# Optimization experiments

Hardware: AMD Instinct MI355X
Metric: run time of the kernel (lower is better)

The kernel has to match this reference:

```python
import jax, jax.numpy as jnp
import numpy as np

C = 1024
GROUPS = 32
EPS = 1e-5
K = 20


def group_norm(v, weight, bias):
    # v: [B, C]; normalize per group of C//GROUPS channels (torch GroupNorm on 2D input)
    B = v.shape[0]
    g = v.reshape(B, GROUPS, C // GROUPS)
    mean = g.mean(axis=-1, keepdims=True)
    var = g.var(axis=-1, keepdims=True)
    g = (g - mean) * jax.lax.rsqrt(var + EPS)
    return g.reshape(B, C) * weight + bias


def setup_inputs() -> dict:
    key = jax.random.key(0)
    ks = jax.random.split(key, 16)
    B, L = 32, 2048
    s = 1.0 / np.sqrt(C)
    inp = {
        "x": jax.random.normal(ks[0], (B, L, C), dtype=jnp.float32),
        "W": jax.random.uniform(ks[1], (C, C), jnp.float32, -s, s),
        "b": jax.random.uniform(ks[2], (C,), jnp.float32, -s, s),
        "W1": jax.random.uniform(ks[3], (C, C), jnp.float32, -s, s),
        "b1": jax.random.uniform(ks[4], (C,), jnp.float32, -s, s),
        "Wm": jax.random.uniform(ks[5], (C, C), jnp.float32, -s, s),
        "bm": jax.random.uniform(ks[6], (C,), jnp.float32, -s, s),
        "Wa": jax.random.uniform(ks[7], (C, C), jnp.float32, -s, s),
        "ba": jax.random.uniform(ks[8], (C,), jnp.float32, -s, s),
        "g1_w": jnp.ones((C,), jnp.float32),
        "g1_b": jnp.zeros((C,), jnp.float32),
        "g2_w": jnp.ones((C,), jnp.float32),
        "g2_b": jnp.zeros((C,), jnp.float32),
    }
    return inp


def reference(x, W, b, W1, b1, Wm, bm, Wa, ba, g1_w, g1_b, g2_w, g2_b):
    # x: [B, L, C]
    x = jnp.einsum('blc,dc->bld', x, W) + b          # self.linear
    x_M = x.mean(axis=1)                              # adaptive avg pool over L -> [B, C]
    x_M = group_norm(x_M @ Wm.T + bm, g1_w, g1_b)     # linear_max + gn1
    x_A = x.max(axis=1)                               # adaptive max pool over L -> [B, C]
    x_A = group_norm(x_A @ Wa.T + ba, g2_w, g2_b)     # linear_Aug + gn2
    x = jnp.einsum('blc,dc->bld', x, W1) + b1         # self.linear1
    out1 = jnp.einsum('blc,bc->bl', x, x_M)           # x @ x_M^T, squeezed
    out2 = jnp.einsum('blc,bc->bl', x, x_A)
    out = jax.nn.softmax(out1, axis=1) * jax.nn.softmax(out2, axis=1)  # [B, L]
    _, topk_idx = jax.lax.top_k(out, K)               # [B, K]
    selected = jnp.take_along_axis(x, topk_idx[:, :, None], axis=1)  # [B, K, C]
    return selected
```

## Files before the change

### kernel.cpp

```cpp
#include <hip/hip_runtime.h>

#define L_SEQ 2048
#define CH    1024
#define NB    32
#define KSEL  20

typedef short v8s  __attribute__((ext_vector_type(8)));
typedef float v16f __attribute__((ext_vector_type(16)));

#define WS_XSUM   0
#define WS_YMAX   32768
#define WS_M1     65536
#define WS_AMAX   98304
#define WS_T1     131072
#define WS_T2     163840
#define WS_P      196608
#define WS_U      262144
#define WS_V      294912
#define WS_S      327680
#define WS_TOPK   393216
#define WS_YSEL   1049216
#define WS_WP     1704576

__device__ __forceinline__ void split8(float4 qa, float4 qb, uint4& hi, uint4& lo) {
  float f[8] = {qa.x, qa.y, qa.z, qa.w, qb.x, qb.y, qb.z, qb.w};
  unsigned h[8], l[8];
  #pragma unroll
  for (int e = 0; e < 8; ++e) {
    unsigned u  = __float_as_uint(f[e]);
    unsigned hu = u & 0xFFFF0000u;
    float lf    = f[e] - __uint_as_float(hu);
    h[e] = u >> 16;
    l[e] = __float_as_uint(lf) >> 16;
  }
  hi.x = h[0] | (h[1] << 16); hi.y = h[2] | (h[3] << 16);
  hi.z = h[4] | (h[5] << 16); hi.w = h[6] | (h[7] << 16);
  lo.x = l[0] | (l[1] << 16); lo.y = l[2] | (l[3] << 16);
  lo.z = l[4] | (l[5] << 16); lo.w = l[6] | (l[7] << 16);
}

__global__ __launch_bounds__(256) void packw_kernel(const float* __restrict__ W,
                                                    uint4* __restrict__ wp,
                                                    float* __restrict__ wsf) {
  int t = threadIdx.x, kt = blockIdx.x, Rw = blockIdx.y;
  int flat = (Rw * 32 + kt) * 256 + t;
  wsf[WS_XSUM + flat] = 0.f;
  wsf[WS_U + flat]    = 0.f;
  const float* wb = W + (size_t)Rw * 128 * CH;
  uint4* out = wp + ((size_t)Rw * 32 + kt) * 1024;
  #pragma unroll
  for (int pass = 0; pass < 2; ++pass) {
    int idx = pass * 256 + t;
    int r = idx >> 2, p = idx & 3;
    const float* ap = wb + (size_t)r * CH + kt * 32 + p * 8;
    float4 f0 = *(const float4*)ap;
    float4 f1 = *(const float4*)(ap + 4);
    uint4 hi, lo;
    split8(f0, f1, hi, lo);
    int slot = ((r >> 5) * 2 + (p >> 1)) * 128 + (p & 1) * 32 + (r & 31);
    out[slot] = hi;
    out[slot + 64] = lo;
  }
}

__global__ __launch_bounds__(256) void mean_kernel(const float* __restrict__ x,
                                                   float* __restrict__ xsum) {
  int b = blockIdx.y, chunk = blockIdx.x, t = threadIdx.x;
  const float4* bp = (const float4*)(x + ((size_t)b * L_SEQ + (size_t)chunk * 64) * CH);
  float sx = 0.f, sy = 0.f, sz = 0.f, sw = 0.f;
  #pragma unroll 4
  for (int l = 0; l < 64; ++l) {
    float4 a = bp[l * 256 + t];
    sx += a.x; sy += a.y; sz += a.z; sw += a.w;
  }
  float* dst = xsum + b * CH + t * 4;
  atomicAdd(dst + 0, sx); atomicAdd(dst + 1, sy);
  atomicAdd(dst + 2, sz); atomicAdd(dst + 3, sw);
}

__global__ __launch_bounds__(256, 2) void gemm_max4(const float* __restrict__ X,
                                                    const uint4* __restrict__ wp,
                                                    unsigned* __restrict__ ymax) {
  __shared__ uint4 smA[2][1024];
  const int t = threadIdx.x, lane = t & 63, w = t >> 6;
  const int wm = w >> 1, wn = w & 1;
  const int blk = blockIdx.x;
  const int strip = blk & 3, mt = blk >> 2;
  const int batch = mt >> 4;
  const float* xb = X + (size_t)mt * 128 * CH;

  const int srow = w * 32 + (lane & 31);
  const int koct = lane >> 5;
  const float* arow = xb + (size_t)srow * CH + koct * 8;

  v16f acc[2][4];
  #pragma unroll
  for (int i = 0; i < 2; ++i)
    #pragma unroll
    for (int j = 0; j < 4; ++j)
      #pragma unroll
      for (int e = 0; e < 16; ++e) acc[i][j][e] = 0.f;

  const uint4* wbB = wp + ((size_t)(strip * 2 + wn)) * 32768 + lane;

  {
    float4 p0 = *(const float4*)(arow);
    float4 p1 = *(const float4*)(arow + 4);
    float4 p2 = *(const float4*)(arow + 16);
    float4 p3 = *(const float4*)(arow + 20);
    uint4 hi, lo;
    split8(p0, p1, hi, lo);
    smA[0][(w * 2 + 0) * 128 + lane] = hi;
    smA[0][(w * 2 + 0) * 128 + 64 + lane] = lo;
    split8(p2, p3, hi, lo);
    smA[0][(w * 2 + 1) * 128 + lane] = hi;
    smA[0][(w * 2 + 1) * 128 + 64 + lane] = lo;
  }
  v8s bc[8], bn[8];
  #pragma unroll
  for (int j = 0; j < 4; ++j) {
    bc[j * 2]     = *(const v8s*)&wbB[((j * 2 + 0) * 2 + 0) * 64];
    bc[j * 2 + 1] = *(const v8s*)&wbB[((j * 2 + 0) * 2 + 1) * 64];
  }
  __syncthreads();

  for (int kt = 0; kt < 32; ++kt) {
    const int cur = kt & 1;
    float4 q0, q1, q2, q3;
    if (kt < 31) {
      const float* an = arow + (kt + 1) * 32;
      q0 = *(const float4*)(an);
      q1 = *(const float4*)(an + 4);
      q2 = *(const float4*)(an + 16);
      q3 = *(const float4*)(an + 20);
    }
    #pragma unroll
    for (int s = 0; s < 2; ++s) {
      const int nkt = s ? kt + 1 : kt, ns = s ^ 1;
      if (nkt < 32) {
        #pragma unroll
        for (int j = 0; j < 4; ++j) {
          bn[j * 2]     = *(const v8s*)&wbB[(size_t)nkt * 1024 + ((j * 2 + ns) * 2 + 0) * 64];
          bn[j * 2 + 1] = *(const v8s*)&wbB[(size_t)nkt * 1024 + ((j * 2 + ns) * 2 + 1) * 64];
        }
      }
      v8s ah[2], al[2];
      #pragma unroll
      for (int i = 0; i < 2; ++i) {
        int base = ((wm * 2 + i) * 2 + s) * 128 + lane;
        ah[i] = *(const v8s*)&smA[cur][base];
        al[i] = *(const v8s*)&smA[cur][base + 64];
      }
      #pragma unroll
      for (int j = 0; j < 4; ++j) {
        v8s bh = bc[j * 2], bl = bc[j * 2 + 1];
        #pragma unroll
        for (int i = 0; i < 2; ++i) {
          acc[i][j] = __builtin_amdgcn_mfma_f32_32x32x16_bf16(ah[i], bh, acc[i][j], 0, 0, 0);
          acc[i][j] = __builtin_amdgcn_mfma_f32_32x32x16_bf16(ah[i], bl, acc[i][j], 0, 0, 0);
          acc[i][j] = __builtin_amdgcn_mfma_f32_32x32x16_bf16(al[i], bh, acc[i][j], 0, 0, 0);
        }
      }
      #pragma unroll
      for (int e = 0; e < 8; ++e) bc[e] = bn[e];
    }
    if (kt < 31) {
      uint4 hi, lo;
      split8(q0, q1, hi, lo);
      smA[cur ^ 1][(w * 2 + 0) * 128 + lane] = hi;
      smA[cur ^ 1][(w * 2 + 0) * 128 + 64 + lane] = lo;
      split8(q2, q3, hi, lo);
      smA[cur ^ 1][(w * 2 + 1) * 128 + lane] = hi;
      smA[cur ^ 1][(w * 2 + 1) * 128 + 64 + lane] = lo;
    }
    __syncthreads();
  }

  #pragma unroll
  for (int j = 0; j < 4; ++j) {
    float m = -INFINITY;
    #pragma unroll
    for (int i = 0; i < 2; ++i)
      #pragma unroll
      for (int e = 0; e < 16; ++e) m = fmaxf(m, acc[i][j][e]);
    m = fmaxf(m, __shfl_xor(m, 32));
    if (lane < 32) {
      int col = strip * 256 + wn * 128 + j * 32 + lane;
      unsigned u = __float_as_uint(m);
      unsigned enc = (m >= 0.f) ? (u | 0x80000000u) : ~u;
      atomicMax(&ymax[batch * CH + col], enc);
    }
  }
}

__global__ __launch_bounds__(256) void poolmix_kernel(const float* __restrict__ xsum,
                                                      const unsigned* __restrict__ ymax,
                                                      const float* __restrict__ W,
                                                      const float* __restrict__ bias,
                                                      float* __restrict__ m1,
                                                      float* __restrict__ amax) {
  int t = threadIdx.x;
  int id = blockIdx.x * 256 + t;
  unsigned u = ymax[id];
  float f = (u & 0x80000000u) ? __uint_as_float(u & 0x7FFFFFFFu) : __uint_as_float(~u);
  amax[id] = f + bias[id & (CH - 1)];

  int d = blockIdx.x * 8 + (t >> 5);
  int b = t & 31;
  const float4* Ir = (const float4*)(xsum + b * CH);
  const float4* Mr = (const float4*)(W + (size_t)d * CH);
  float acc = 0.f;
  #pragma unroll 4
  for (int c = 0; c < CH / 4; ++c) {
    float4 a = Ir[c], m = Mr[c];
    acc += a.x * m.x + a.y * m.y + a.z * m.z + a.w * m.w;
  }
  m1[b * CH + d] = acc * (1.f / 2048.f) + bias[d];
}

__global__ __launch_bounds__(256) void lin2_kernel(const float* __restrict__ m1,
                                                   const float* __restrict__ amax,
                                                   const float* __restrict__ Wm,
                                                   const float* __restrict__ bm,
                                                   const float* __restrict__ Wa,
                                                   const float* __restrict__ ba,
                                                   float* __restrict__ t1,
                                                   float* __restrict__ t2) {
  int t = threadIdx.x;
  int which = blockIdx.x >> 7, bk = blockIdx.x & 127;
  const float* I = which ? amax : m1;
  const float* M = which ? Wa : Wm;
  const float* bb = which ? ba : bm;
  float* O = which ? t2 : t1;
  int d = bk * 8 + (t >> 5);
  int b = t & 31;
  const float4* Ir = (const float4*)(I + b * CH);
  const float4* Mr = (const float4*)(M + (size_t)d * CH);
  float acc = 0.f;
  #pragma unroll 4
  for (int c = 0; c < CH / 4; ++c) {
    float4 a = Ir[c], m = Mr[c];
    acc += a.x * m.x + a.y * m.y + a.z * m.z + a.w * m.w;
  }
  O[b * CH + d] = acc + bb[d];
}

__global__ __launch_bounds__(1024) void gnp_kernel(const float* __restrict__ t1,
                                                   const float* __restrict__ t2,
                                                   const float* __restrict__ g1w, const float* __restrict__ g1b,
                                                   const float* __restrict__ g2w, const float* __restrict__ g2b,
                                                   float* __restrict__ p) {
  int b = blockIdx.x, c = threadIdx.x;
  float v1 = t1[b * CH + c], v2 = t2[b * CH + c];
  float s1 = v1, s2 = v2;
  #pragma unroll
  for (int off = 16; off; off >>= 1) { s1 += __shfl_xor(s1, off); s2 += __shfl_xor(s2, off); }
  float d1 = v1 - s1 * (1.f / 32.f), d2 = v2 - s2 * (1.f / 32.f);
  float q1 = d1 * d1, q2 = d2 * d2;
  #pragma unroll
  for (int off = 16; off; off >>= 1) { q1 += __shfl_xor(q1, off); q2 += __shfl_xor(q2, off); }
  float o1 = d1 * rsqrtf(q1 * (1.f / 32.f) + 1e-5f) * g1w[c] + g1b[c];
  float o2 = d2 * rsqrtf(q2 * (1.f / 32.f) + 1e-5f) * g2w[c] + g2b[c];
  p[b * CH + c] = o1 + o2;
}

__global__ __launch_bounds__(256) void colmm_kernel(const float* __restrict__ S,
                                                    const float* __restrict__ M,
                                                    float* __restrict__ O) {
  __shared__ float Sl[128][32];
  int t = threadIdx.x;
  int e0 = (blockIdx.x & 3) * 256, c0 = (blockIdx.x >> 2) * 128;
  for (int i = t; i < 4096; i += 256) {
    int c = i >> 5, b = i & 31;
    Sl[c][b] = S[b * CH + c0 + c];
  }
  __syncthreads();
  int e = e0 + t;
  float acc[32];
  #pragma unroll
  for (int b = 0; b < 32; ++b) acc[b] = 0.f;
  for (int c = 0; c < 128; ++c) {
    float wv = M[(size_t)(c0 + c) * CH + e];
    #pragma unroll
    for (int b = 0; b < 32; ++b) acc[b] += Sl[c][b] * wv;
  }
  #pragma unroll
  for (int b = 0; b < 32; ++b) atomicAdd(&O[b * CH + e], acc[b]);
}

__global__ __launch_bounds__(256) void logits_kernel(const float* __restrict__ x,
                                                     const float* __restrict__ v,
                                                     float* __restrict__ s) {
  __shared__ float4 vl[256];
  int b = blockIdx.y, chunk = blockIdx.x, t = threadIdx.x;
  vl[t] = ((const float4*)(v + b * CH))[t];
  __syncthreads();
  int wv = t >> 6, lane = t & 63;
  for (int it = 0; it < 8; ++it) {
    int l = chunk * 32 + it * 4 + wv;
    const float4* xr = (const float4*)(x + ((size_t)b * L_SEQ + l) * CH);
    float acc = 0.f;
    #pragma unroll
    for (int rep = 0; rep < 4; ++rep) {
      float4 a = xr[rep * 64 + lane];
      float4 c = vl[rep * 64 + lane];
      acc += a.x * c.x + a.y * c.y + a.z * c.z + a.w * c.w;
    }
    #pragma unroll
    for (int off = 32; off; off >>= 1) acc += __shfl_xor(acc, off);
    if (lane == 0) s[b * L_SEQ + l] = acc;
  }
}

__global__ __launch_bounds__(256) void topk_kernel(const float* __restrict__ s,
                                                   int* __restrict__ idx_out) {
  int b = blockIdx.x, t = threadIdx.x;
  int lane = t & 63, w = t >> 6;
  __shared__ float lv[4];
  __shared__ int   li[4];
  float v[8];
  #pragma unroll
  for (int j = 0; j < 8; ++j) v[j] = s[b * L_SEQ + j * 256 + t];
  for (int k = 0; k < KSEL; ++k) {
    float bv = -INFINITY; int bi = 1 << 30;
    #pragma unroll
    for (int j = 0; j < 8; ++j) {
      int gi = j * 256 + t;
      if (v[j] > bv || (v[j] == bv && gi < bi)) { bv = v[j]; bi = gi; }
    }
    #pragma unroll
    for (int off = 32; off; off >>= 1) {
      float ov = __shfl_xor(bv, off); int oi = __shfl_xor(bi, off);
      if (ov > bv || (ov == bv && oi < bi)) { bv = ov; bi = oi; }
    }
    if (lane == 0) { lv[w] = bv; li[w] = bi; }
    __syncthreads();
    float fv = lv[0]; int fi = li[0];
    #pragma unroll
    for (int w2 = 1; w2 < 4; ++w2) {
      float ov = lv[w2]; int oi = li[w2];
      if (ov > fv || (ov == fv && oi < fi)) { fv = ov; fi = oi; }
    }
    if (t == 0) idx_out[b * KSEL + k] = fi;
    if ((fi & 255) == t) v[fi >> 8] = -INFINITY;
    __syncthreads();
  }
}

__global__ __launch_bounds__(256) void selgemm_idx_kernel(const float* __restrict__ X,
                                                          const int* __restrict__ idx,
                                                          const float* __restrict__ B,
                                                          const float* __restrict__ bias,
                                                          float* __restrict__ C) {
  __shared__ float As[64][17];
  __shared__ float Bs[64][17];
  __shared__ int rmap[64];
  int t = threadIdx.x;
  int tx = t & 15, ty = t >> 4;
  int n0 = blockIdx.x * 64, m0 = blockIdx.y * 64;
  if (t < 64) {
    int rr = m0 + t;
    rmap[t] = (rr / KSEL) * L_SEQ + idx[rr];
  }
  __syncthreads();
  float acc[4][4];
  #pragma unroll
  for (int i = 0; i < 4; ++i)
    #pragma unroll
    for (int j = 0; j < 4; ++j) acc[i][j] = 0.f;
  for (int k0 = 0; k0 < CH; k0 += 16) {
    #pragma unroll
    for (int j = 0; j < 4; ++j) {
      int e = t * 4 + j;
      int row = e >> 4, kk = e & 15;
      As[row][kk] = X[(size_t)rmap[row] * CH + k0 + kk];
      Bs[row][kk] = B[(size_t)(n0 + row) * CH + k0 + kk];
    }
    __syncthreads();
    #pragma unroll
    for (int kk = 0; kk < 16; ++kk) {
      float a[4], bb[4];
      #pragma unroll
      for (int i = 0; i < 4; ++i) a[i] = As[ty * 4 + i][kk];
      #pragma unroll
      for (int j = 0; j < 4; ++j) bb[j] = Bs[tx * 4 + j][kk];
      #pragma unroll
      for (int i = 0; i < 4; ++i)
        #pragma unroll
        for (int j = 0; j < 4; ++j) acc[i][j] += a[i] * bb[j];
    }
    __syncthreads();
  }
  #pragma unroll
  for (int i = 0; i < 4; ++i)
    #pragma unroll
    for (int j = 0; j < 4; ++j)
      C[(size_t)(m0 + ty * 4 + i) * CH + n0 + tx * 4 + j] = acc[i][j] + bias[n0 + tx * 4 + j];
}

__global__ __launch_bounds__(256) void selgemm_kernel(const float* __restrict__ A,
                                                      const float* __restrict__ B,
                                                      const float* __restrict__ bias,
                                                      float* __restrict__ C) {
  __shared__ float As[64][17];
  __shared__ float Bs[64][17];
  int t = threadIdx.x;
  int tx = t & 15, ty = t >> 4;
  int n0 = blockIdx.x * 64, m0 = blockIdx.y * 64;
  float acc[4][4];
  #pragma unroll
  for (int i = 0; i < 4; ++i)
    #pragma unroll
    for (int j = 0; j < 4; ++j) acc[i][j] = 0.f;
  for (int k0 = 0; k0 < CH; k0 += 16) {
    #pragma unroll
    for (int j = 0; j < 4; ++j) {
      int e = t * 4 + j;
      int row = e >> 4, kk = e & 15;
      As[row][kk] = A[(size_t)(m0 + row) * CH + k0 + kk];
      Bs[row][kk] = B[(size_t)(n0 + row) * CH + k0 + kk];
    }
    __syncthreads();
    #pragma unroll
    for (int kk = 0; kk < 16; ++kk) {
      float a[4], bb[4];
      #pragma unroll
      for (int i = 0; i < 4; ++i) a[i] = As[ty * 4 + i][kk];
      #pragma unroll
      for (int j = 0; j < 4; ++j) bb[j] = Bs[tx * 4 + j][kk];
      #pragma unroll
      for (int i = 0; i < 4; ++i)
        #pragma unroll
        for (int j = 0; j < 4; ++j) acc[i][j] += a[i] * bb[j];
    }
    __syncthreads();
  }
  #pragma unroll
  for (int i = 0; i < 4; ++i)
    #pragma unroll
    for (int j = 0; j < 4; ++j)
      C[(size_t)(m0 + ty * 4 + i) * CH + n0 + tx * 4 + j] = acc[i][j] + bias[n0 + tx * 4 + j];
}

extern "C" void kernel_launch(void* const* d_in, const int* in_sizes, int n_in,
                              void* d_out, int out_size, void* d_ws, size_t ws_size,
                              hipStream_t stream) {
  const float* x   = (const float*)d_in[0];
  const float* W   = (const float*)d_in[1];
  const float* b   = (const float*)d_in[2];
  const float* W1  = (const float*)d_in[3];
  const float* b1  = (const float*)d_in[4];
  const float* Wm  = (const float*)d_in[5];
  const float* bm  = (const float*)d_in[6];
  const float* Wa  = (const float*)d_in[7];
  const float* ba  = (const float*)d_in[8];
  const float* g1w = (const float*)d_in[9];
  const float* g1b = (const float*)d_in[10];
  const float* g2w = (const float*)d_in[11];
  const float* g2b = (const float*)d_in[12];

  float* wsf = (float*)d_ws;
  float*    xsum = wsf + WS_XSUM;
  unsigned* ymax = (unsigned*)(wsf + WS_YMAX);
  float*    m1   = wsf + WS_M1;
  float*    amax = wsf + WS_AMAX;
  float*    t1   = wsf + WS_T1;
  float*    t2   = wsf + WS_T2;
  float*    p    = wsf + WS_P;
  float*    u    = wsf + WS_U;
  float*    vvec = wsf + WS_V;
  float*    sbuf = wsf + WS_S;
  int*      tidx = (int*)(wsf + WS_TOPK);
  float*    Ysel = wsf + WS_YSEL;
  uint4*    wpak = (uint4*)(wsf + WS_WP);

  packw_kernel<<<dim3(32, 8), 256, 0, stream>>>(W, wpak, wsf);
  mean_kernel<<<dim3(32, 32), 256, 0, stream>>>(x, xsum);
  gemm_max4<<<2048, 256, 0, stream>>>(x, wpak, ymax);

  poolmix_kernel<<<128, 256, 0, stream>>>(xsum, ymax, W, b, m1, amax);
  lin2_kernel<<<256, 256, 0, stream>>>(m1, amax, Wm, bm, Wa, ba, t1, t2);
  gnp_kernel<<<32, 1024, 0, stream>>>(t1, t2, g1w, g1b, g2w, g2b, p);
  colmm_kernel<<<32, 256, 0, stream>>>(p, W1, u);
  colmm_kernel<<<32, 256, 0, stream>>>(u, W, vvec);
  logits_kernel<<<dim3(64, 32), 256, 0, stream>>>(x, vvec, sbuf);
  topk_kernel<<<32, 256, 0, stream>>>(sbuf, tidx);
  selgemm_idx_kernel<<<dim3(16, 10), 256, 0, stream>>>(x, tidx, W, b, Ysel);
  selgemm_kernel<<<dim3(16, 10), 256, 0, stream>>>(Ysel, W1, b1, (float*)d_out);
}
```

Measured before the change: 1.098 ms.

## Fold W1·W into one combined weight and use MFMA for selected-row GEMM

After: 1.045 ms. -4.8%, faster.

```diff
diff --git a/kernel.cpp b/kernel.cpp
--- a/kernel.cpp
+++ b/kernel.cpp
@@ -15,12 +15,13 @@
 #define WS_T1     131072
 #define WS_T2     163840
 #define WS_P      196608
-#define WS_U      262144
 #define WS_V      294912
 #define WS_S      327680
 #define WS_TOPK   393216
-#define WS_YSEL   1049216
-#define WS_WP     1704576
+#define WS_BC     394240
+#define WS_WC     395264
+#define WS_WPAK   1443840
+#define WS_WTPAK  2492416
 
 __device__ __forceinline__ void split8(float4 qa, float4 qb, uint4& hi, uint4& lo) {
   float f[8] = {qa.x, qa.y, qa.z, qa.w, qb.x, qb.y, qb.z, qb.w};
@@ -41,11 +42,13 @@
 
 __global__ __launch_bounds__(256) void packw_kernel(const float* __restrict__ W,
                                                     uint4* __restrict__ wp,
-                                                    float* __restrict__ wsf) {
+                                                    float* __restrict__ zws) {
   int t = threadIdx.x, kt = blockIdx.x, Rw = blockIdx.y;
-  int flat = (Rw * 32 + kt) * 256 + t;
-  wsf[WS_XSUM + flat] = 0.f;
-  wsf[WS_U + flat]    = 0.f;
+  if (zws) {
+    int flat = (Rw * 32 + kt) * 256 + t;
+    zws[WS_XSUM + flat] = 0.f;
+    if (flat < 32768) zws[WS_V + flat] = 0.f;
+  }
   const float* wb = W + (size_t)Rw * 128 * CH;
   uint4* out = wp + ((size_t)Rw * 32 + kt) * 1024;
   #pragma unroll
@@ -63,6 +66,34 @@
   }
 }
 
+__global__ __launch_bounds__(256) void packwt_kernel(const float* __restrict__ W,
+                                                     uint4* __restrict__ wtp) {
+  __shared__ float Wl[32][129];
+  int t = threadIdx.x, kt = blockIdx.x, cc = blockIdx.y;
+  #pragma unroll
+  for (int it = 0; it < 16; ++it) {
+    int idx = it * 256 + t;
+    int el = idx >> 7, cl = idx & 127;
+    Wl[el][cl] = W[(size_t)(kt * 32 + el) * CH + cc * 128 + cl];
+  }
+  __syncthreads();
+  uint4* out = wtp + ((size_t)cc * 32 + kt) * 1024;
+  #pragma unroll
+  for (int pass = 0; pass < 2; ++pass) {
+    int sid = pass * 256 + t;
+    int r = sid >> 2, p = sid & 3;
+    float f[8];
+    #pragma unroll
+    for (int q = 0; q < 8; ++q) f[q] = Wl[p * 8 + q][r];
+    float4 f0 = {f[0], f[1], f[2], f[3]}, f1 = {f[4], f[5], f[6], f[7]};
+    uint4 hi, lo;
+    split8(f0, f1, hi, lo);
+    int slot = ((r >> 5) * 2 + (p >> 1)) * 128 + (p & 1) * 32 + (r & 31);
+    out[slot] = hi;
+    out[slot + 64] = lo;
+  }
+}
+
 __global__ __launch_bounds__(256) void mean_kernel(const float* __restrict__ x,
                                                    float* __restrict__ xsum) {
   int b = blockIdx.y, chunk = blockIdx.x, t = threadIdx.x;
@@ -78,31 +109,13 @@
   atomicAdd(dst + 2, sz); atomicAdd(dst + 3, sw);
 }
 
-__global__ __launch_bounds__(256, 2) void gemm_max4(const float* __restrict__ X,
-                                                    const uint4* __restrict__ wp,
-                                                    unsigned* __restrict__ ymax) {
-  __shared__ uint4 smA[2][1024];
-  const int t = threadIdx.x, lane = t & 63, w = t >> 6;
-  const int wm = w >> 1, wn = w & 1;
-  const int blk = blockIdx.x;
-  const int strip = blk & 3, mt = blk >> 2;
-  const int batch = mt >> 4;
-  const float* xb = X + (size_t)mt * 128 * CH;
-
-  const int srow = w * 32 + (lane & 31);
-  const int koct = lane >> 5;
-  const float* arow = xb + (size_t)srow * CH + koct * 8;
-
-  v16f acc[2][4];
-  #pragma unroll
-  for (int i = 0; i < 2; ++i)
-    #pragma unroll
-    for (int j = 0; j < 4; ++j)
-      #pragma unroll
-      for (int e = 0; e < 16; ++e) acc[i][j][e] = 0.f;
-
-  const uint4* wbB = wp + ((size_t)(strip * 2 + wn)) * 32768 + lane;
-
+template<bool FOURTH>
+__device__ __forceinline__ void gemm_core(const float* __restrict__ arow,
+                                          const uint4* __restrict__ wbB,
+                                          const int cgbase,
+                                          uint4 (*__restrict__ smA)[1024],
+                                          const int w, const int lane,
+                                          v16f acc[4][2]) {
   {
     float4 p0 = *(const float4*)(arow);
     float4 p1 = *(const float4*)(arow + 4);
@@ -116,11 +129,11 @@
     smA[0][(w * 2 + 1) * 128 + lane] = hi;
     smA[0][(w * 2 + 1) * 128 + 64 + lane] = lo;
   }
-  v8s bc[8], bn[8];
-  #pragma unroll
-  for (int j = 0; j < 4; ++j) {
-    bc[j * 2]     = *(const v8s*)&wbB[((j * 2 + 0) * 2 + 0) * 64];
-    bc[j * 2 + 1] = *(const v8s*)&wbB[((j * 2 + 0) * 2 + 1) * 64];
+  v8s bc[4], bn[4];
+  #pragma unroll
+  for (int j = 0; j < 2; ++j) {
+    bc[j * 2]     = *(const v8s*)&wbB[((cgbase + j) * 2 + 0) * 128];
+    bc[j * 2 + 1] = *(const v8s*)&wbB[((cgbase + j) * 2 + 0) * 128 + 64];
   }
   __syncthreads();
 
@@ -139,30 +152,32 @@
       const int nkt = s ? kt + 1 : kt, ns = s ^ 1;
       if (nkt < 32) {
         #pragma unroll
-        for (int j = 0; j < 4; ++j) {
-          bn[j * 2]     = *(const v8s*)&wbB[(size_t)nkt * 1024 + ((j * 2 + ns) * 2 + 0) * 64];
-          bn[j * 2 + 1] = *(const v8s*)&wbB[(size_t)nkt * 1024 + ((j * 2 + ns) * 2 + 1) * 64];
+        for (int j = 0; j < 2; ++j) {
+          bn[j * 2]     = *(const v8s*)&wbB[(size_t)nkt * 1024 + ((cgbase + j) * 2 + ns) * 128];
+          bn[j * 2 + 1] = *(const v8s*)&wbB[(size_t)nkt * 1024 + ((cgbase + j) * 2 + ns) * 128 + 64];
         }
       }
-      v8s ah[2], al[2];
-      #pragma unroll
-      for (int i = 0; i < 2; ++i) {
-        int base = ((wm * 2 + i) * 2 + s) * 128 + lane;
+      v8s ah[4], al[4];
+      #pragma unroll
+      for (int i = 0; i < 4; ++i) {
+        int base = (i * 2 + s) * 128 + lane;
         ah[i] = *(const v8s*)&smA[cur][base];
         al[i] = *(const v8s*)&smA[cur][base + 64];
       }
       #pragma unroll
-      for (int j = 0; j < 4; ++j) {
+      for (int j = 0; j < 2; ++j) {
         v8s bh = bc[j * 2], bl = bc[j * 2 + 1];
         #pragma unroll
-        for (int i = 0; i < 2; ++i) {
+        for (int i = 0; i < 4; ++i) {
           acc[i][j] = __builtin_amdgcn_mfma_f32_32x32x16_bf16(ah[i], bh, acc[i][j], 0, 0, 0);
           acc[i][j] = __builtin_amdgcn_mfma_f32_32x32x16_bf16(ah[i], bl, acc[i][j], 0, 0, 0);
           acc[i][j] = __builtin_amdgcn_mfma_f32_32x32x16_bf16(al[i], bh, acc[i][j], 0, 0, 0);
+          if (FOURTH)
+            acc[i][j] = __builtin_amdgcn_mfma_f32_32x32x16_bf16(al[i], bl, acc[i][j], 0, 0, 0);
         }
       }
       #pragma unroll
-      for (int e = 0; e < 8; ++e) bc[e] = bn[e];
+      for (int e = 0; e < 4; ++e) bc[e] = bn[e];
     }
     if (kt < 31) {
       uint4 hi, lo;
@@ -175,22 +190,128 @@
     }
     __syncthreads();
   }
-
-  #pragma unroll
-  for (int j = 0; j < 4; ++j) {
+}
+
+__global__ __launch_bounds__(256, 2) void gemm_max5(const float* __restrict__ X,
+                                                    const uint4* __restrict__ wp,
+                                                    unsigned* __restrict__ ymax) {
+  __shared__ uint4 smA[2][1024];
+  const int t = threadIdx.x, lane = t & 63, w = t >> 6;
+  const int blk = blockIdx.x;
+  const int strip = blk & 3, mt = blk >> 2;
+  const int batch = mt >> 4;
+  const float* arow = X + (size_t)(mt * 128 + w * 32 + (lane & 31)) * CH + (lane >> 5) * 8;
+  v16f acc[4][2];
+  #pragma unroll
+  for (int i = 0; i < 4; ++i)
+    #pragma unroll
+    for (int j = 0; j < 2; ++j)
+      #pragma unroll
+      for (int e = 0; e < 16; ++e) acc[i][j][e] = 0.f;
+  const uint4* wbB = wp + (size_t)(strip * 2 + (w >> 1)) * 32768 + lane;
+  gemm_core<false>(arow, wbB, (w & 1) * 2, smA, w, lane, acc);
+
+  #pragma unroll
+  for (int j = 0; j < 2; ++j) {
     float m = -INFINITY;
     #pragma unroll
-    for (int i = 0; i < 2; ++i)
+    for (int i = 0; i < 4; ++i)
       #pragma unroll
       for (int e = 0; e < 16; ++e) m = fmaxf(m, acc[i][j][e]);
     m = fmaxf(m, __shfl_xor(m, 32));
     if (lane < 32) {
-      int col = strip * 256 + wn * 128 + j * 32 + lane;
+      int col = strip * 256 + w * 64 + j * 32 + lane;
       unsigned u = __float_as_uint(m);
       unsigned enc = (m >= 0.f) ? (u | 0x80000000u) : ~u;
       atomicMax(&ymax[batch * CH + col], enc);
     }
   }
+}
+
+__global__ __launch_bounds__(256, 2) void wc_gemm(const float* __restrict__ W1,
+                                                  const uint4* __restrict__ wtp,
+                                                  float* __restrict__ Wc) {
+  __shared__ uint4 smA[2][1024];
+  const int t = threadIdx.x, lane = t & 63, w = t >> 6;
+  const int blk = blockIdx.x;
+  const int strip = blk & 3, mt = blk >> 2;
+  const float* arow = W1 + (size_t)(mt * 128 + w * 32 + (lane & 31)) * CH + (lane >> 5) * 8;
+  v16f acc[4][2];
+  #pragma unroll
+  for (int i = 0; i < 4; ++i)
+    #pragma unroll
+    for (int j = 0; j < 2; ++j)
+      #pragma unroll
+      for (int e = 0; e < 16; ++e) acc[i][j][e] = 0.f;
+  const uint4* wbB = wtp + (size_t)(strip * 2 + (w >> 1)) * 32768 + lane;
+  gemm_core<true>(arow, wbB, (w & 1) * 2, smA, w, lane, acc);
+
+  #pragma unroll
+  for (int i = 0; i < 4; ++i)
+    #pragma unroll
+    for (int j = 0; j < 2; ++j)
+      #pragma unroll
+      for (int r = 0; r < 16; ++r) {
+        int row = (r & 3) + 8 * (r >> 2) + 4 * (lane >> 5);
+        int grow = mt * 128 + i * 32 + row;
+        int gcol = strip * 256 + w * 64 + j * 32 + (lane & 31);
+        Wc[(size_t)grow * CH + gcol] = acc[i][j][r];
+      }
+}
+
+__global__ __launch_bounds__(256, 2) void out_gemm(const float* __restrict__ X,
+                                                   const int* __restrict__ idx,
+                                                   const uint4* __restrict__ wcp,
+                                                   const float* __restrict__ bc,
+                                                   float* __restrict__ C) {
+  __shared__ uint4 smA[2][1024];
+  const int t = threadIdx.x, lane = t & 63, w = t >> 6;
+  const int blk = blockIdx.x;
+  const int strip = blk & 3, mt = blk >> 2;
+  const int rr = mt * 128 + w * 32 + (lane & 31);
+  const int grow_a = (rr / KSEL) * L_SEQ + idx[rr];
+  const float* arow = X + (size_t)grow_a * CH + (lane >> 5) * 8;
+  v16f acc[4][2];
+  #pragma unroll
+  for (int i = 0; i < 4; ++i)
+    #pragma unroll
+    for (int j = 0; j < 2; ++j)
+      #pragma unroll
+      for (int e = 0; e < 16; ++e) acc[i][j][e] = 0.f;
+  const uint4* wbB = wcp + (size_t)(strip * 2 + (w >> 1)) * 32768 + lane;
+  gemm_core<true>(arow, wbB, (w & 1) * 2, smA, w, lane, acc);
+
+  #pragma unroll
+  for (int i = 0; i < 4; ++i)
+    #pragma unroll
+    for (int j = 0; j < 2; ++j)
+      #pragma unroll
+      for (int r = 0; r < 16; ++r) {
+        int row = (r & 3) + 8 * (r >> 2) + 4 * (lane >> 5);
+        int grow = mt * 128 + i * 32 + row;
+        int gcol = strip * 256 + w * 64 + j * 32 + (lane & 31);
+        C[(size_t)grow * CH + gcol] = acc[i][j][r] + bc[gcol];
+      }
+}
+
+__global__ __launch_bounds__(256) void bc_kernel(const float* __restrict__ W1,
+                                                 const float* __restrict__ b,
+                                                 const float* __restrict__ b1,
+                                                 float* __restrict__ bc) {
+  int t = threadIdx.x;
+  int d = blockIdx.x * 8 + (t >> 5);
+  int lane = t & 31;
+  const float4* wr = (const float4*)(W1 + (size_t)d * CH);
+  const float4* br = (const float4*)b;
+  float acc = 0.f;
+  #pragma unroll
+  for (int c = lane; c < 256; c += 32) {
+    float4 a = wr[c], m = br[c];
+    acc += a.x * m.x + a.y * m.y + a.z * m.z + a.w * m.w;
+  }
+  #pragma unroll
+  for (int off = 16; off; off >>= 1) acc += __shfl_xor(acc, off);
+  if (lane == 0) bc[d] = acc + b1[d];
 }
 
 __global__ __launch_bounds__(256) void poolmix_kernel(const float* __restrict__ xsum,
@@ -347,101 +468,6 @@
   }
 }
 
-__global__ __launch_bounds__(256) void selgemm_idx_kernel(const float* __restrict__ X,
-                                                          const int* __restrict__ idx,
-                                                          const float* __restrict__ B,
-                                                          const float* __restrict__ bias,
-                                                          float* __restrict__ C) {
-  __shared__ float As[64][17];
-  __shared__ float Bs[64][17];
-  __shared__ int rmap[64];
-  int t = threadIdx.x;
-  int tx = t & 15, ty = t >> 4;
-  int n0 = blockIdx.x * 64, m0 = blockIdx.y * 64;
-  if (t < 64) {
-    int rr = m0 + t;
-    rmap[t] = (rr / KSEL) * L_SEQ + idx[rr];
-  }
-  __syncthreads();
-  float acc[4][4];
-  #pragma unroll
-  for (int i = 0; i < 4; ++i)
-    #pragma unroll
-    for (int j = 0; j < 4; ++j) acc[i][j] = 0.f;
-  for (int k0 = 0; k0 < CH; k0 += 16) {
-    #pragma unroll
-    for (int j = 0; j < 4; ++j) {
-      int e = t * 4 + j;
-      int row = e >> 4, kk = e & 15;
-      As[row][kk] = X[(size_t)rmap[row] * CH + k0 + kk];
-      Bs[row][kk] = B[(size_t)(n0 + row) * CH + k0 + kk];
-    }
-    __syncthreads();
-    #pragma unroll
-    for (int kk = 0; kk < 16; ++kk) {
-      float a[4], bb[4];
-      #pragma unroll
-      for (int i = 0; i < 4; ++i) a[i] = As[ty * 4 + i][kk];
-      #pragma unroll
-      for (int j = 0; j < 4; ++j) bb[j] = Bs[tx * 4 + j][kk];
-      #pragma unroll
-      for (int i = 0; i < 4; ++i)
-        #pragma unroll
-        for (int j = 0; j < 4; ++j) acc[i][j] += a[i] * bb[j];
-    }
-    __syncthreads();
-  }
-  #pragma unroll
-  for (int i = 0; i < 4; ++i)
-    #pragma unroll
-    for (int j = 0; j < 4; ++j)
-      C[(size_t)(m0 + ty * 4 + i) * CH + n0 + tx * 4 + j] = acc[i][j] + bias[n0 + tx * 4 + j];
-}
-
-__global__ __launch_bounds__(256) void selgemm_kernel(const float* __restrict__ A,
-                                                      const float* __restrict__ B,
-                                                      const float* __restrict__ bias,
-                                                      float* __restrict__ C) {
-  __shared__ float As[64][17];
-  __shared__ float Bs[64][17];
-  int t = threadIdx.x;
-  int tx = t & 15, ty = t >> 4;
-  int n0 = blockIdx.x * 64, m0 = blockIdx.y * 64;
-  float acc[4][4];
-  #pragma unroll
-  for (int i = 0; i < 4; ++i)
-    #pragma unroll
-    for (int j = 0; j < 4; ++j) acc[i][j] = 0.f;
-  for (int k0 = 0; k0 < CH; k0 += 16) {
-    #pragma unroll
-    for (int j = 0; j < 4; ++j) {
-      int e = t * 4 + j;
-      int row = e >> 4, kk = e & 15;
-      As[row][kk] = A[(size_t)(m0 + row) * CH + k0 + kk];
-      Bs[row][kk] = B[(size_t)(n0 + row) * CH + k0 + kk];
-    }
-    __syncthreads();
-    #pragma unroll
-    for (int kk = 0; kk < 16; ++kk) {
-      float a[4], bb[4];
-      #pragma unroll
-      for (int i = 0; i < 4; ++i) a[i] = As[ty * 4 + i][kk];
-      #pragma unroll
-      for (int j = 0; j < 4; ++j) bb[j] = Bs[tx * 4 + j][kk];
-      #pragma unroll
-      for (int i = 0; i < 4; ++i)
-        #pragma unroll
-        for (int j = 0; j < 4; ++j) acc[i][j] += a[i] * bb[j];
-    }
-    __syncthreads();
-  }
-  #pragma unroll
-  for (int i = 0; i < 4; ++i)
-    #pragma unroll
-    for (int j = 0; j < 4; ++j)
-      C[(size_t)(m0 + ty * 4 + i) * CH + n0 + tx * 4 + j] = acc[i][j] + bias[n0 + tx * 4 + j];
-}
-
 extern "C" void kernel_launch(void* const* d_in, const int* in_sizes, int n_in,
                               void* d_out, int out_size, void* d_ws, size_t ws_size,
                               hipStream_t stream) {
@@ -467,24 +493,28 @@
   float*    t1   = wsf + WS_T1;
   float*    t2   = wsf + WS_T2;
   float*    p    = wsf + WS_P;
-  float*    u    = wsf + WS_U;
   float*    vvec = wsf + WS_V;
   float*    sbuf = wsf + WS_S;
   int*      tidx = (int*)(wsf + WS_TOPK);
-  float*    Ysel = wsf + WS_YSEL;
-  uint4*    wpak = (uint4*)(wsf + WS_WP);
+  float*    bcv  = wsf + WS_BC;
+  float*    Wc   = wsf + WS_WC;
+  uint4*    wpak = (uint4*)(wsf + WS_WPAK);
+  uint4*    wtpak = (uint4*)(wsf + WS_WTPAK);
 
   packw_kernel<<<dim3(32, 8), 256, 0, stream>>>(W, wpak, wsf);
+  packwt_kernel<<<dim3(32, 8), 256, 0, stream>>>(W, wtpak);
   mean_kernel<<<dim3(32, 32), 256, 0, stream>>>(x, xsum);
-  gemm_max4<<<2048, 256, 0, stream>>>(x, wpak, ymax);
+  gemm_max5<<<2048, 256, 0, stream>>>(x, wpak, ymax);
+
+  wc_gemm<<<32, 256, 0, stream>>>(W1, wtpak, Wc);
+  bc_kernel<<<128, 256, 0, stream>>>(W1, b, b1, bcv);
+  packw_kernel<<<dim3(32, 8), 256, 0, stream>>>(Wc, wtpak, nullptr);
 
   poolmix_kernel<<<128, 256, 0, stream>>>(xsum, ymax, W, b, m1, amax);
   lin2_kernel<<<256, 256, 0, stream>>>(m1, amax, Wm, bm, Wa, ba, t1, t2);
   gnp_kernel<<<32, 1024, 0, stream>>>(t1, t2, g1w, g1b, g2w, g2b, p);
-  colmm_kernel<<<32, 256, 0, stream>>>(p, W1, u);
-  colmm_kernel<<<32, 256, 0, stream>>>(u, W, vvec);
+  colmm_kernel<<<32, 256, 0, stream>>>(p, Wc, vvec);
   logits_kernel<<<dim3(64, 32), 256, 0, stream>>>(x, vvec, sbuf);
   topk_kernel<<<32, 256, 0, stream>>>(sbuf, tidx);
-  selgemm_idx_kernel<<<dim3(16, 10), 256, 0, stream>>>(x, tidx, W, b, Ysel);
-  selgemm_kernel<<<dim3(16, 10), 256, 0, stream>>>(Ysel, W1, b1, (float*)d_out);
-}
+  out_gemm<<<20, 256, 0, stream>>>(x, tidx, wtpak, bcv, (float*)d_out);
+}
```
